# Kernel tuning notes

Hardware: AMD Instinct MI355X
Metric: run time of the kernel (lower is better)

Reference implementation:

```python
import jax, jax.numpy as jnp
import numpy as np
from jax import lax
from jax.scipy.linalg import expm
from jax.scipy.special import logsumexp

V, D, S, C, A, H = 1024, 2, 256, 16, 4, 64
ITERS, LR, CLIP = 4, 0.1, 1.0
EPS = 1e-12


def setup_inputs() -> dict:
    key = jax.random.key(0)
    ks = jax.random.split(key, 8)
    return {
        "children1_VxD": jax.random.normal(ks[0], (V, D), jnp.float32),
        "children2_VxD": jax.random.normal(ks[1], (V, D), jnp.float32),
        "log_felsensteins1_VxSxA": jax.nn.log_softmax(jax.random.normal(ks[2], (V, S, A), jnp.float32), -1),
        "log_felsensteins2_VxSxA": jax.nn.log_softmax(jax.random.normal(ks[3], (V, S, A), jnp.float32), -1),
        "site_positions_SxC": jax.random.uniform(ks[4], (S, C), jnp.float32),
        "W1": jax.random.normal(ks[5], (D + C, H), jnp.float32) * 0.2,
        "b1": jnp.zeros((H,), jnp.float32),
        "Wq": jax.random.normal(ks[6], (H, A * A), jnp.float32) * 0.2,
        "bq": jnp.zeros((A * A,), jnp.float32),
        "Wp": jax.random.normal(ks[7], (H, A), jnp.float32) * 0.2,
        "bp": jnp.zeros((A,), jnp.float32),
    }


def _safe_norm(x_VxD):
    # safe_norm(x, dim=1, keepdim=True)
    return jnp.sqrt(jnp.sum(x_VxD * x_VxD, axis=1, keepdims=True) + EPS)


def _decode(parents_VxD, site_positions_SxC, W1, b1, Wq, bq, Wp, bp):
    # QMatrixDecoder: per-(V,S) valid rate matrix + stationary probs from a small MLP.
    v, d = parents_VxD.shape
    s, c = site_positions_SxC.shape
    feat_VxSxF = jnp.concatenate([
        jnp.broadcast_to(parents_VxD[:, None, :], (v, s, d)),
        jnp.broadcast_to(site_positions_SxC[None, :, :], (v, s, c)),
    ], axis=-1)
    h_VxSxH = jax.nn.relu(feat_VxSxF @ W1 + b1)
    rates_VxSxAxA = jax.nn.softplus(h_VxSxH @ Wq + bq).reshape(v, s, A, A)
    eye = jnp.eye(A, dtype=rates_VxSxAxA.dtype)
    off = rates_VxSxAxA * (1.0 - eye)
    Q_VxSxAxA = off - eye * jnp.sum(off, axis=-1, keepdims=True)  # rows sum to 0
    stat_probs_VxSxA = jax.nn.softmax(h_VxSxH @ Wp + bp, axis=-1)
    return Q_VxSxAxA, stat_probs_VxSxA


def _log_felsenstein(Q_VxSxAxA, lf1_VxSxA, lf2_VxSxA, branch1_V, branch2_V):
    def one(lf_VxSxA, branch_V):
        P_VxSxAxA = expm(Q_VxSxAxA * branch_V[:, None, None, None])
        logP = jnp.log(jnp.clip(P_VxSxAxA, 1e-30, None))
        # log(P @ fels): logsumexp over child state b of logP[..., a, b] + lf[..., b]
        return logsumexp(logP + lf_VxSxA[:, :, None, :], axis=-1)
    return one(lf1_VxSxA, branch1_V) + one(lf2_VxSxA, branch2_V)


def _forward(children1_VxD, children2_VxD, lf1_VxSxA, lf2_VxSxA, site_positions_SxC, W1, b1, Wq, bq, Wp, bp):
    c1 = lax.stop_gradient(children1_VxD)
    c2 = lax.stop_gradient(children2_VxD)
    lf1 = lax.stop_gradient(lf1_VxSxA)
    lf2 = lax.stop_gradient(lf2_VxSxA)
    sp = lax.stop_gradient(site_positions_SxC)

    pn = _safe_norm(c1)
    qn = _safe_norm(c2)
    p = jnp.where(pn > qn, c1 * qn / pn, c1)
    q = jnp.where(qn > pn, c2 * pn / qn, c2)
    v = c1.shape[0]

    def loglik(alpha_V, beta_V):
        midpoints = p * alpha_V[:, None] + q * (1.0 - alpha_V[:, None])
        parents = midpoints * beta_V[:, None]
        # Q matrix and stat probs are .detach()ed in the original: no grad through decoder.
        Q, stat = _decode(lax.stop_gradient(parents), sp, W1, b1, Wq, bq, Wp, bp)
        branch1 = jnp.sqrt(jnp.sum((c1 - parents) ** 2, axis=-1) + EPS)
        branch2 = jnp.sqrt(jnp.sum((c2 - parents) ** 2, axis=-1) + EPS)
        lf = _log_felsenstein(Q, lf1, lf2, branch1, branch2)
        ll_VxS = logsumexp(lf + jnp.log(stat), axis=-1)
        # backward(ones) on independent per-V scalars == grad of the sum
        return jnp.sum(ll_VxS), parents

    grad_fn = jax.grad(loglik, argnums=(0, 1), has_aux=True)

    def step(carry, _):
        alpha, beta = carry
        (ga, gb), parents = grad_fn(alpha, beta)
        alpha = jnp.clip(alpha + LR * jnp.clip(ga, -CLIP, CLIP), 0.0, 1.0)
        beta = jnp.clip(beta + LR * jnp.clip(gb, -CLIP, CLIP), 0.0, 1.0)
        return (alpha, beta), parents

    init = (jnp.full((v,), 0.5, c1.dtype), jnp.full((v,), 0.5, c1.dtype))
    _, parents_seq = lax.scan(step, init, None, length=ITERS)
    # original returns parents from the last iteration (pre-update alpha/beta), detached
    return lax.stop_gradient(parents_seq[-1])


def reference(children1_VxD, children2_VxD, log_felsensteins1_VxSxA, log_felsensteins2_VxSxA, site_positions_SxC, W1, b1, Wq, bq, Wp, bp):
    return _forward(children1_VxD, children2_VxD, log_felsensteins1_VxSxA, log_felsensteins2_VxSxA,
                    site_positions_SxC, W1, b1, Wq, bq, Wp, bp)
```

## Files before the change

kernel.cpp:

```cpp
#include <hip/hip_runtime.h>
#include <math.h>

#define EPSf 1e-12f

typedef float v2f __attribute__((ext_vector_type(2)));
typedef float f32x4 __attribute__((ext_vector_type(4)));
typedef _Float16 f16x8 __attribute__((ext_vector_type(8)));

__device__ __forceinline__ v2f mkv2(float a, float b) { v2f r; r.x = a; r.y = b; return r; }

__device__ __forceinline__ v2f pk_fma(v2f a, v2f b, v2f c) {
  v2f d; asm("v_pk_fma_f32 %0, %1, %2, %3" : "=v"(d) : "v"(a), "v"(b), "v"(c)); return d;
}
__device__ __forceinline__ v2f pk_mul(v2f a, v2f b) {
  v2f d; asm("v_pk_mul_f32 %0, %1, %2" : "=v"(d) : "v"(a), "v"(b)); return d;
}
__device__ __forceinline__ v2f v2max(v2f a, v2f b) { return __builtin_elementwise_max(a, b); }
__device__ __forceinline__ v2f pk_fma_bl(v2f a, v2f b, v2f c) {
  v2f d; asm("v_pk_fma_f32 %0, %1, %2, %3 op_sel:[0,0,0] op_sel_hi:[0,1,1]"
             : "=v"(d) : "v"(a), "v"(b), "v"(c)); return d;
}
__device__ __forceinline__ v2f pk_fma_bh(v2f a, v2f b, v2f c) {
  v2f d; asm("v_pk_fma_f32 %0, %1, %2, %3 op_sel:[1,0,0] op_sel_hi:[1,1,1]"
             : "=v"(d) : "v"(a), "v"(b), "v"(c)); return d;
}
__device__ __forceinline__ v2f pk_mul_bl(v2f a, v2f b) {
  v2f d; asm("v_pk_mul_f32 %0, %1, %2 op_sel:[0,0] op_sel_hi:[0,1]"
             : "=v"(d) : "v"(a), "v"(b)); return d;
}

__device__ __forceinline__ void mm4v(v2f* C, const v2f* X, const v2f* Y) {
#pragma unroll
  for (int i = 0; i < 4; ++i) {
    v2f x01 = X[2*i], x23 = X[2*i+1];
#pragma unroll
    for (int jp = 0; jp < 2; ++jp) {
      v2f acc = pk_mul_bl(x01, Y[0 + jp]);
      acc = pk_fma_bh(x01, Y[2 + jp], acc);
      acc = pk_fma_bl(x23, Y[4 + jp], acc);
      acc = pk_fma_bh(x23, Y[6 + jp], acc);
      C[2*i + jp] = acc;
    }
  }
}
__device__ __forceinline__ void mm4v_acc(v2f* C, const v2f* X, const v2f* Y) {
#pragma unroll
  for (int i = 0; i < 4; ++i) {
    v2f x01 = X[2*i], x23 = X[2*i+1];
#pragma unroll
    for (int jp = 0; jp < 2; ++jp) {
      v2f acc = C[2*i + jp];
      acc = pk_fma_bl(x01, Y[0 + jp], acc);
      acc = pk_fma_bh(x01, Y[2 + jp], acc);
      acc = pk_fma_bl(x23, Y[4 + jp], acc);
      acc = pk_fma_bh(x23, Y[6 + jp], acc);
      C[2*i + jp] = acc;
    }
  }
}

__device__ __forceinline__ void site_branch(const v2f* Qm, const v2f* Q2, const v2f* Q3,
                                            const v2f* Q4, float Lmax, float t,
                                            const float* f, float* y, float* dy) {
  float r = Lmax * t * 0.66666667f;
  int m = 0;
  if (r > 1.f) {
    unsigned u = __float_as_uint(r);
    m = (int)(u >> 23) - 127 + (((u & 0x7fffffu) != 0u) ? 1 : 0);
  }
  const float tau = t * __uint_as_float((unsigned)(127 - m) << 23);
  const float t2s = tau * tau, t3s = t2s * tau, t4s = t2s * t2s;
  const v2f tc = mkv2(tau, t2s * 0.5f);
  const float d0 = t4s * (1.f/24.f);
  const v2f cc = mkv2(t3s * (1.f/6.f), d0);
  const v2f dA = mkv2(t4s * tau * (1.f/120.f), t4s * t2s * (1.f/720.f));
  const v2f dB = mkv2(t4s * t3s * (1.f/5040.f), t4s * t4s * (1.f/40320.f));

  v2f T[8], C1[8];
#pragma unroll
  for (int ip = 0; ip < 8; ++ip) {
    v2f a = pk_mul_bl(cc, Q3[ip]);
    a = pk_fma_bh(tc, Q2[ip], a);
    T[ip] = pk_fma_bl(tc, Qm[ip], a);
    v2f b = pk_mul_bl(dA, Qm[ip]);
    b = pk_fma_bh(dA, Q2[ip], b);
    b = pk_fma_bl(dB, Q3[ip], b);
    C1[ip] = pk_fma_bh(dB, Q4[ip], b);
  }
  T[0].x += 1.f;  T[2].y += 1.f;  T[5].x += 1.f;  T[7].y += 1.f;
  C1[0].x += d0;  C1[2].y += d0;  C1[5].x += d0;  C1[7].y += d0;
  mm4v_acc(T, Q4, C1);

  for (int k = 0; k < m; ++k) {
    v2f S[8];
    mm4v(S, T, T);
#pragma unroll
    for (int ip = 0; ip < 8; ++ip) T[ip] = S[ip];
  }

  const v2f f01 = mkv2(f[0], f[1]), f23 = mkv2(f[2], f[3]);
  const v2f lo = mkv2(1e-30f, 1e-30f);
#pragma unroll
  for (int i = 0; i < 4; ++i) {
    v2f a = pk_mul(v2max(T[2*i], lo), f01);
    a = pk_fma(v2max(T[2*i+1], lo), f23, a);
    y[i] = a.x + a.y;
  }
  const v2f y01 = mkv2(y[0], y[1]), y23 = mkv2(y[2], y[3]);
#pragma unroll
  for (int i = 0; i < 4; ++i) {
    v2f a = pk_mul(Qm[2*i], y01);
    a = pk_fma(Qm[2*i+1], y23, a);
    dy[i] = a.x + a.y;
  }
}

__device__ __forceinline__ int cmapf(int c) { return 5*(c >> 2) + 1 + (c & 3); }

__global__ __launch_bounds__(256) void prep_kernel(
    const float* __restrict__ spg, const float* __restrict__ W1g,
    const float* __restrict__ b1g, const float* __restrict__ Wqg,
    const float* __restrict__ bqg, const float* __restrict__ Wpg,
    const float* __restrict__ bpg,
    _Float16* __restrict__ U0h,
    f16x8* __restrict__ W1Alo, f16x8* __restrict__ W1Ahi,
    f16x8* __restrict__ W1Blo, f16x8* __restrict__ W1Bhi,
    f16x8* __restrict__ WBlo,  f16x8* __restrict__ WBhi,
    float* __restrict__ bias16)
{
  const int jp = blockIdx.x;
  const int s  = threadIdx.x;
  const int j0 = 2*jp, j1 = 2*jp + 1;
  float u0 = b1g[j0], u1 = b1g[j1];
#pragma unroll
  for (int k4 = 0; k4 < 4; ++k4) {
    float4 v4 = reinterpret_cast<const float4*>(spg)[s*4 + k4];
    const float* W0 = W1g + (2 + 4*k4)*64;
    u0 = fmaf(v4.x, W0[j0],       u0);  u1 = fmaf(v4.x, W0[j1],       u1);
    u0 = fmaf(v4.y, W0[64 + j0],  u0);  u1 = fmaf(v4.y, W0[64 + j1],  u1);
    u0 = fmaf(v4.z, W0[128 + j0], u0);  u1 = fmaf(v4.z, W0[128 + j1], u1);
    u0 = fmaf(v4.w, W0[192 + j0], u0);  u1 = fmaf(v4.w, W0[192 + j1], u1);
  }
  U0h[s*64 + j0] = (_Float16)u0;
  U0h[s*64 + j1] = (_Float16)u1;

  if (jp == 0 && s < 64) {
    const int k0 = (s >> 4) * 8;
    f16x8 alo, ahi, blo, bhi;
#pragma unroll
    for (int j = 0; j < 8; ++j) {
      alo[j] = (_Float16)W1g[k0 + j];
      ahi[j] = (_Float16)W1g[32 + k0 + j];
      blo[j] = (_Float16)W1g[64 + k0 + j];
      bhi[j] = (_Float16)W1g[96 + k0 + j];
    }
    W1Alo[s] = alo; W1Ahi[s] = ahi; W1Blo[s] = blo; W1Bhi[s] = bhi;
  }
  if (jp == 1 && s < 64) {
    const int col = s & 15;
    const int k0 = (s >> 4) * 8;
    f16x8 wlo, whi;
#pragma unroll
    for (int j = 0; j < 8; ++j) {
      float vlo, vhi;
      if (col < 12) { vlo = Wqg[(k0 + j)*16 + cmapf(col)];  vhi = Wqg[(32 + k0 + j)*16 + cmapf(col)]; }
      else          { vlo = Wpg[(k0 + j)*4 + (col - 12)];   vhi = Wpg[(32 + k0 + j)*4 + (col - 12)]; }
      wlo[j] = (_Float16)vlo; whi[j] = (_Float16)vhi;
    }
    WBlo[s] = wlo; WBhi[s] = whi;
  }
  if (jp == 2 && s < 16) {
    bias16[s] = (s < 12) ? bqg[cmapf(s)] : bpg[s - 12];
  }
}

__global__ __launch_bounds__(256) void mlme_kernel(
    const float* __restrict__ c1g, const float* __restrict__ c2g,
    const float* __restrict__ lf1g, const float* __restrict__ lf2g,
    const _Float16* __restrict__ U0h,
    const f16x8* __restrict__ W1Alo, const f16x8* __restrict__ W1Ahi,
    const f16x8* __restrict__ W1Blo, const f16x8* __restrict__ W1Bhi,
    const f16x8* __restrict__ WBlo,  const f16x8* __restrict__ WBhi,
    const float* __restrict__ bias16g,
    float* __restrict__ outg)
{
  __shared__ float cLDS[256 * 20];
  __shared__ float sred[24];

  const int v = blockIdx.x;
  const int tid = threadIdx.x;
  const int lane = tid & 63;
  const int wid = tid >> 6;
  const int lane16 = lane & 15;
  const int kgrp = lane >> 4;

  const f16x8 w1alo = W1Alo[lane], w1ahi = W1Ahi[lane];
  const f16x8 w1blo = W1Blo[lane], w1bhi = W1Bhi[lane];
  const f16x8 wblo  = WBlo[lane],  wbhi  = WBhi[lane];

  const float c10 = c1g[2*v], c11 = c1g[2*v+1];
  const float c20 = c2g[2*v], c21 = c2g[2*v+1];
  float p0, p1, q0, q1;
  {
    float pn = sqrtf(c10*c10 + c11*c11 + EPSf);
    float qn = sqrtf(c20*c20 + c21*c21 + EPSf);
    p0 = c10; p1 = c11; q0 = c20; q1 = c21;
    if (pn > qn) { float rr = qn/pn; p0 = c10*rr; p1 = c11*rr; }
    if (qn > pn) { float rr = pn/qn; q0 = c20*rr; q1 = c21*rr; }
  }
  float alpha = 0.5f, beta = 0.5f;

  float f1[4], f2[4];
  {
    float4 a = reinterpret_cast<const float4*>(lf1g)[v*256 + tid];
    float4 b = reinterpret_cast<const float4*>(lf2g)[v*256 + tid];
    f1[0]=__expf(a.x); f1[1]=__expf(a.y); f1[2]=__expf(a.z); f1[3]=__expf(a.w);
    f2[0]=__expf(b.x); f2[1]=__expf(b.y); f2[2]=__expf(b.z); f2[3]=__expf(b.w);
  }

  const _Float16* Ubase = U0h + (wid*64 + lane16)*64 + kgrp*8;

  for (int it = 0; it < 3; ++it) {
    const float mid0 = p0*alpha + q0*(1.f-alpha);
    const float mid1 = p1*alpha + q1*(1.f-alpha);
    const float par0 = mid0*beta, par1 = mid1*beta;
    const float d10 = c10-par0, d11 = c11-par1;
    const float d20 = c20-par0, d21 = c21-par1;
    const float t1 = sqrtf(d10*d10 + d11*d11 + EPSf);
    const float t2 = sqrtf(d20*d20 + d21*d21 + EPSf);

    const _Float16 p0h = (_Float16)par0, p1h = (_Float16)par1;
    const f16x8 p0v = {p0h,p0h,p0h,p0h,p0h,p0h,p0h,p0h};
    const f16x8 p1v = {p1h,p1h,p1h,p1h,p1h,p1h,p1h,p1h};
    const f16x8 z8 = {0,0,0,0,0,0,0,0};
    f32x4 accm[4];
#pragma unroll
    for (int mt = 0; mt < 4; ++mt) {
      accm[mt] = (f32x4){0.f, 0.f, 0.f, 0.f};
      f16x8 ulo = *reinterpret_cast<const f16x8*>(Ubase + mt*16*64);
      f16x8 uhi = *reinterpret_cast<const f16x8*>(Ubase + mt*16*64 + 32);
      f16x8 hlo = __builtin_elementwise_max(
          __builtin_elementwise_fma(p1v, w1blo, __builtin_elementwise_fma(p0v, w1alo, ulo)), z8);
      f16x8 hhi = __builtin_elementwise_max(
          __builtin_elementwise_fma(p1v, w1bhi, __builtin_elementwise_fma(p0v, w1ahi, uhi)), z8);
      accm[mt] = __builtin_amdgcn_mfma_f32_16x16x32_f16(hlo, wblo, accm[mt], 0, 0, 0);
      accm[mt] = __builtin_amdgcn_mfma_f32_16x16x32_f16(hhi, wbhi, accm[mt], 0, 0, 0);
    }
#pragma unroll
    for (int mt = 0; mt < 4; ++mt) {
#pragma unroll
      for (int i = 0; i < 4; ++i) {
        cLDS[(wid*64 + mt*16 + kgrp*4 + i)*20 + lane16] = accm[mt][i];
      }
    }
    __syncthreads();
    float a16[16];
#pragma unroll
    for (int cg = 0; cg < 4; ++cg) {
      f32x4 vv = *reinterpret_cast<const f32x4*>(&cLDS[tid*20 + cg*4]);
#pragma unroll
      for (int i = 0; i < 4; ++i) a16[cg*4 + i] = vv[i] + bias16g[cg*4 + i];
    }

    float o[12];
#pragma unroll
    for (int k = 0; k < 12; ++k) {
      float xx = a16[k];
      o[k] = fmaxf(xx, 0.f) + __logf(1.f + __expf(-fabsf(xx)));
    }
    const float rs0 = o[0]+o[1]+o[2],  rs1 = o[3]+o[4]+o[5];
    const float rs2 = o[6]+o[7]+o[8],  rs3 = o[9]+o[10]+o[11];
    v2f Qm[8];
    Qm[0] = mkv2(-rs0, o[0]);  Qm[1] = mkv2(o[1], o[2]);
    Qm[2] = mkv2(o[3], -rs1);  Qm[3] = mkv2(o[4], o[5]);
    Qm[4] = mkv2(o[6], o[7]);  Qm[5] = mkv2(-rs2, o[8]);
    Qm[6] = mkv2(o[9], o[10]); Qm[7] = mkv2(o[11], -rs3);
    const float cs0 = rs0 + o[3] + o[6] + o[9];
    const float cs1 = o[0] + rs1 + o[7] + o[10];
    const float cs2 = o[1] + o[4] + rs2 + o[11];
    const float cs3 = o[2] + o[5] + o[8] + rs3;
    const float L1Q = fmaxf(fmaxf(cs0, cs1), fmaxf(cs2, cs3));
    float Lmax = L1Q;
#pragma unroll
    for (int off = 1; off < 64; off <<= 1)
      Lmax = fmaxf(Lmax, __shfl_xor(Lmax, off, 64));

    float st[4];
    {
      float mx = fmaxf(fmaxf(a16[12], a16[13]), fmaxf(a16[14], a16[15]));
      st[0]=__expf(a16[12]-mx); st[1]=__expf(a16[13]-mx);
      st[2]=__expf(a16[14]-mx); st[3]=__expf(a16[15]-mx);
    }

    v2f Q2m[8], Q3m[8], Q4m[8];
    mm4v(Q2m, Qm, Qm);
    mm4v(Q3m, Q2m, Qm);
    mm4v(Q4m, Q2m, Q2m);

    float y1[4], dy1[4], y2[4], dy2[4];
    site_branch(Qm, Q2m, Q3m, Q4m, Lmax, t1, f1, y1, dy1);
    site_branch(Qm, Q2m, Q3m, Q4m, Lmax, t2, f2, y2, dy2);

    float den = 0.f, num1 = 0.f, num2 = 0.f;
#pragma unroll
    for (int a = 0; a < 4; ++a) {
      float ys2 = y2[a] * st[a];
      den  = fmaf(y1[a],  ys2, den);
      num1 = fmaf(dy1[a], ys2, num1);
      num2 = fmaf(y1[a] * st[a], dy2[a], num2);
    }
    const float invden = 1.f / den;
    float g1c = num1 * invden;
    float g2c = num2 * invden;

#pragma unroll
    for (int off = 32; off > 0; off >>= 1) {
      g1c += __shfl_xor(g1c, off, 64);
      g2c += __shfl_xor(g2c, off, 64);
    }
    if (lane == 0) { sred[it*8 + wid*2 + 0] = g1c; sred[it*8 + wid*2 + 1] = g2c; }
    __syncthreads();
    {
      float g1 = sred[it*8+0]+sred[it*8+2]+sred[it*8+4]+sred[it*8+6];
      float g2 = sred[it*8+1]+sred[it*8+3]+sred[it*8+5]+sred[it*8+7];
      float db1da = ((par0-c10)*(p0-q0) + (par1-c11)*(p1-q1)) * beta / t1;
      float db2da = ((par0-c20)*(p0-q0) + (par1-c21)*(p1-q1)) * beta / t2;
      float db1db = ((par0-c10)*mid0 + (par1-c11)*mid1) / t1;
      float db2db = ((par0-c20)*mid0 + (par1-c21)*mid1) / t2;
      float ga = g1*db1da + g2*db2da;
      float gb = g1*db1db + g2*db2db;
      ga = fminf(1.f, fmaxf(-1.f, ga));
      gb = fminf(1.f, fmaxf(-1.f, gb));
      alpha = fminf(1.f, fmaxf(0.f, alpha + 0.1f*ga));
      beta  = fminf(1.f, fmaxf(0.f, beta  + 0.1f*gb));
    }
  }

  if (tid == 0) {
    float m0 = p0*alpha + q0*(1.f-alpha);
    float m1 = p1*alpha + q1*(1.f-alpha);
    outg[2*v]   = m0*beta;
    outg[2*v+1] = m1*beta;
  }
}

extern "C" void kernel_launch(void* const* d_in, const int* in_sizes, int n_in,
                              void* d_out, int out_size, void* d_ws, size_t ws_size,
                              hipStream_t stream) {
  (void)in_sizes; (void)n_in; (void)ws_size; (void)out_size;
  const float* c1  = (const float*)d_in[0];
  const float* c2  = (const float*)d_in[1];
  const float* lf1 = (const float*)d_in[2];
  const float* lf2 = (const float*)d_in[3];
  const float* sp  = (const float*)d_in[4];
  const float* W1  = (const float*)d_in[5];
  const float* b1  = (const float*)d_in[6];
  const float* Wq  = (const float*)d_in[7];
  const float* bq  = (const float*)d_in[8];
  const float* Wp  = (const float*)d_in[9];
  const float* bp  = (const float*)d_in[10];
  float* out = (float*)d_out;

  char* ws = (char*)d_ws;
  _Float16* U0h   = (_Float16*)ws;
  f16x8* W1Alo = (f16x8*)(ws + 32768);
  f16x8* W1Ahi = (f16x8*)(ws + 33792);
  f16x8* W1Blo = (f16x8*)(ws + 34816);
  f16x8* W1Bhi = (f16x8*)(ws + 35840);
  f16x8* WBlo  = (f16x8*)(ws + 36864);
  f16x8* WBhi  = (f16x8*)(ws + 37888);
  float* bias16 = (float*)(ws + 38912);

  prep_kernel<<<dim3(32), dim3(256), 0, stream>>>(sp, W1, b1, Wq, bq, Wp, bp,
                                                  U0h, W1Alo, W1Ahi, W1Blo, W1Bhi,
                                                  WBlo, WBhi, bias16);
  mlme_kernel<<<dim3(1024), dim3(256), 0, stream>>>(
      c1, c2, lf1, lf2, U0h, W1Alo, W1Ahi, W1Blo, W1Bhi, WBlo, WBhi, bias16, out);
}
```

Measured before the change: 43.54 us.

## Share squaring count across branches, fold bias into MFMA, drop block barrier

```diff
diff --git a/kernel.cpp b/kernel.cpp
--- a/kernel.cpp
+++ b/kernel.cpp
@@ -59,24 +59,15 @@
   }
 }
 
-__device__ __forceinline__ void site_branch(const v2f* Qm, const v2f* Q2, const v2f* Q3,
-                                            const v2f* Q4, float Lmax, float t,
-                                            const float* f, float* y, float* dy) {
-  float r = Lmax * t * 0.66666667f;
-  int m = 0;
-  if (r > 1.f) {
-    unsigned u = __float_as_uint(r);
-    m = (int)(u >> 23) - 127 + (((u & 0x7fffffu) != 0u) ? 1 : 0);
-  }
-  const float tau = t * __uint_as_float((unsigned)(127 - m) << 23);
+__device__ __forceinline__ void taylor8(v2f* T, const v2f* Qm, const v2f* Q2,
+                                        const v2f* Q3, const v2f* Q4, float tau) {
   const float t2s = tau * tau, t3s = t2s * tau, t4s = t2s * t2s;
   const v2f tc = mkv2(tau, t2s * 0.5f);
   const float d0 = t4s * (1.f/24.f);
   const v2f cc = mkv2(t3s * (1.f/6.f), d0);
   const v2f dA = mkv2(t4s * tau * (1.f/120.f), t4s * t2s * (1.f/720.f));
   const v2f dB = mkv2(t4s * t3s * (1.f/5040.f), t4s * t4s * (1.f/40320.f));
-
-  v2f T[8], C1[8];
+  v2f C1[8];
 #pragma unroll
   for (int ip = 0; ip < 8; ++ip) {
     v2f a = pk_mul_bl(cc, Q3[ip]);
@@ -90,14 +81,10 @@
   T[0].x += 1.f;  T[2].y += 1.f;  T[5].x += 1.f;  T[7].y += 1.f;
   C1[0].x += d0;  C1[2].y += d0;  C1[5].x += d0;  C1[7].y += d0;
   mm4v_acc(T, Q4, C1);
-
-  for (int k = 0; k < m; ++k) {
-    v2f S[8];
-    mm4v(S, T, T);
-#pragma unroll
-    for (int ip = 0; ip < 8; ++ip) T[ip] = S[ip];
-  }
-
+}
+
+__device__ __forceinline__ void ydy(const v2f* Qm, const v2f* T, const float* f,
+                                    float* y, float* dy) {
   const v2f f01 = mkv2(f[0], f[1]), f23 = mkv2(f[2], f[3]);
   const v2f lo = mkv2(1e-30f, 1e-30f);
 #pragma unroll
@@ -113,6 +100,34 @@
     a = pk_fma(Qm[2*i+1], y23, a);
     dy[i] = a.x + a.y;
   }
+}
+
+__device__ __forceinline__ void site_branch_pair(
+    const v2f* Qm, const v2f* Q2, const v2f* Q3, const v2f* Q4,
+    float Lmax, float t1, float t2, const float* f1, const float* f2,
+    float* y1, float* dy1, float* y2, float* dy2)
+{
+  float r = Lmax * fmaxf(t1, t2) * 0.66666667f;
+  int m = 0;
+  if (r > 1.f) {
+    unsigned u = __float_as_uint(r);
+    m = (int)(u >> 23) - 127 + (((u & 0x7fffffu) != 0u) ? 1 : 0);
+  }
+  const float sc = __uint_as_float((unsigned)(127 - m) << 23);
+
+  v2f T1[8], T2[8];
+  taylor8(T1, Qm, Q2, Q3, Q4, t1 * sc);
+  taylor8(T2, Qm, Q2, Q3, Q4, t2 * sc);
+
+  for (int k = 0; k < m; ++k) {
+    v2f S1[8], S2[8];
+    mm4v(S1, T1, T1);
+    mm4v(S2, T2, T2);
+#pragma unroll
+    for (int ip = 0; ip < 8; ++ip) { T1[ip] = S1[ip]; T2[ip] = S2[ip]; }
+  }
+  ydy(Qm, T1, f1, y1, dy1);
+  ydy(Qm, T2, f2, y2, dy2);
 }
 
 __device__ __forceinline__ int cmapf(int c) { return 5*(c >> 2) + 1 + (c & 3); }
@@ -194,10 +209,6 @@
   const int lane16 = lane & 15;
   const int kgrp = lane >> 4;
 
-  const f16x8 w1alo = W1Alo[lane], w1ahi = W1Ahi[lane];
-  const f16x8 w1blo = W1Blo[lane], w1bhi = W1Bhi[lane];
-  const f16x8 wblo  = WBlo[lane],  wbhi  = WBhi[lane];
-
   const float c10 = c1g[2*v], c11 = c1g[2*v+1];
   const float c20 = c2g[2*v], c21 = c2g[2*v+1];
   float p0, p1, q0, q1;
@@ -218,6 +229,8 @@
     f2[0]=__expf(b.x); f2[1]=__expf(b.y); f2[2]=__expf(b.z); f2[3]=__expf(b.w);
   }
 
+  const float biasv = bias16g[lane16];
+
   const _Float16* Ubase = U0h + (wid*64 + lane16)*64 + kgrp*8;
 
   for (int it = 0; it < 3; ++it) {
@@ -229,6 +242,10 @@
     const float t1 = sqrtf(d10*d10 + d11*d11 + EPSf);
     const float t2 = sqrtf(d20*d20 + d21*d21 + EPSf);
 
+    const f16x8 w1alo = W1Alo[lane], w1ahi = W1Ahi[lane];
+    const f16x8 w1blo = W1Blo[lane], w1bhi = W1Bhi[lane];
+    const f16x8 wblo  = WBlo[lane],  wbhi  = WBhi[lane];
+
     const _Float16 p0h = (_Float16)par0, p1h = (_Float16)par1;
     const f16x8 p0v = {p0h,p0h,p0h,p0h,p0h,p0h,p0h,p0h};
     const f16x8 p1v = {p1h,p1h,p1h,p1h,p1h,p1h,p1h,p1h};
@@ -236,7 +253,7 @@
     f32x4 accm[4];
 #pragma unroll
     for (int mt = 0; mt < 4; ++mt) {
-      accm[mt] = (f32x4){0.f, 0.f, 0.f, 0.f};
+      accm[mt] = (f32x4){biasv, biasv, biasv, biasv};
       f16x8 ulo = *reinterpret_cast<const f16x8*>(Ubase + mt*16*64);
       f16x8 uhi = *reinterpret_cast<const f16x8*>(Ubase + mt*16*64 + 32);
       f16x8 hlo = __builtin_elementwise_max(
@@ -253,13 +270,14 @@
         cLDS[(wid*64 + mt*16 + kgrp*4 + i)*20 + lane16] = accm[mt][i];
       }
     }
-    __syncthreads();
+    asm volatile("s_waitcnt lgkmcnt(0)" ::: "memory");
+    __builtin_amdgcn_sched_barrier(0);
     float a16[16];
 #pragma unroll
     for (int cg = 0; cg < 4; ++cg) {
       f32x4 vv = *reinterpret_cast<const f32x4*>(&cLDS[tid*20 + cg*4]);
 #pragma unroll
-      for (int i = 0; i < 4; ++i) a16[cg*4 + i] = vv[i] + bias16g[cg*4 + i];
+      for (int i = 0; i < 4; ++i) a16[cg*4 + i] = vv[i];
     }
 
     float o[12];
@@ -298,8 +316,7 @@
     mm4v(Q4m, Q2m, Q2m);
 
     float y1[4], dy1[4], y2[4], dy2[4];
-    site_branch(Qm, Q2m, Q3m, Q4m, Lmax, t1, f1, y1, dy1);
-    site_branch(Qm, Q2m, Q3m, Q4m, Lmax, t2, f2, y2, dy2);
+    site_branch_pair(Qm, Q2m, Q3m, Q4m, Lmax, t1, t2, f1, f2, y1, dy1, y2, dy2);
 
     float den = 0.f, num1 = 0.f, num2 = 0.f;
 #pragma unroll
```

Result: slower. 45.22 us (+3.9%).
